# Kernel tuning notes

Hardware: AMD Instinct MI355X
Metric: run time of the kernel (lower is better)

Reference implementation:

```python
import jax, jax.numpy as jnp
import numpy as np

H = 16  # n_heads
D = 64  # d_keys


def setup_inputs() -> dict:
    key = jax.random.key(0)
    ks = jax.random.split(key, 11)
    b, n, dm = 2, 2048, 1024
    s = 1.0 / np.sqrt(dm)
    return {
        "q": jax.random.normal(ks[0], (b, n, dm), jnp.float32),
        "k": jax.random.normal(ks[1], (b, n, dm), jnp.float32),
        "v": jax.random.normal(ks[2], (b, n, dm), jnp.float32),
        "Wq": jax.random.normal(ks[3], (dm, H * D), jnp.float32) * s,
        "bq": jax.random.normal(ks[4], (H * D,), jnp.float32) * 0.01,
        "Wk": jax.random.normal(ks[5], (dm, H * D), jnp.float32) * s,
        "bk": jax.random.normal(ks[6], (H * D,), jnp.float32) * 0.01,
        "Wv": jax.random.normal(ks[7], (dm, H * D), jnp.float32) * s,
        "bv": jax.random.normal(ks[8], (H * D,), jnp.float32) * 0.01,
        "Wo": jax.random.normal(ks[9], (H * D, dm), jnp.float32) * s,
        "bo": jax.random.normal(ks[10], (dm,), jnp.float32) * 0.01,
    }


def reference(q, k, v, Wq, bq, Wk, bk, Wv, bv, Wo, bo):
    b, n_q, _ = q.shape
    n_k = k.shape[1]
    # projections -> [b, n, h, d]
    qh = (q @ Wq + bq).reshape(b, n_q, H, D)
    kh = (k @ Wk + bk).reshape(b, n_k, H, D)
    vh = (v @ Wv + bv).reshape(b, n_k, H, D)
    # scores [b, h, n, m]
    scores = jnp.einsum('bnhd,bmhd->bhnm', qh, kh)
    causal = jnp.triu(jnp.ones((n_q, n_k), dtype=bool), k=1)  # True above diag
    scores = jnp.where(causal, -jnp.inf, scores)
    att = jax.nn.softmax(scores / np.sqrt(D).astype(np.float32), axis=-1)
    att_out = jnp.einsum('bhnm,bmhd->bnhd', att, vh).reshape(b, n_q, H * D)
    return att_out @ Wo + bo
```

## Files before the change

### kernel.cpp

```cpp
#include <hip/hip_runtime.h>

typedef float f32x4 __attribute__((ext_vector_type(4)));
typedef __bf16 bf16x8 __attribute__((ext_vector_type(8)));
typedef __bf16 bf16x4 __attribute__((ext_vector_type(4)));
typedef __bf16 bf16_t;

#define NH 16
#define DH 64
#define SEQ 2048
#define DM 1024

extern "C" hipError_t hipMemPtrGetInfo(void* ptr, size_t* size);

__device__ __forceinline__ bf16x8 ld8(const bf16_t* p) { return *(const bf16x8*)p; }
__device__ __forceinline__ void st8(bf16_t* p, bf16x8 v) { *(bf16x8*)p = v; }

__device__ __forceinline__ void gl_lds16(const bf16_t* g, bf16_t* l)
{
    __builtin_amdgcn_global_load_lds(
        (const __attribute__((address_space(1))) unsigned int*)g,
        (__attribute__((address_space(3))) unsigned int*)l, 16, 0, 0);
}

__global__ __launch_bounds__(256) void fill_sentinel(float* out, unsigned n, float val)
{
    unsigned stride = gridDim.x * blockDim.x;
    for (unsigned i = blockIdx.x * blockDim.x + threadIdx.x; i < n; i += stride)
        out[i] = val;
}

__global__ __launch_bounds__(256) void prep(
    const float* __restrict__ q, const float* __restrict__ k,
    const float* __restrict__ v,
    const float* __restrict__ w0, const float* __restrict__ w1,
    const float* __restrict__ w2, const float* __restrict__ w3,
    bf16_t* __restrict__ xb, bf16_t* __restrict__ wt)
{
    int z = blockIdx.z;
    if (z < 3) {
        const float* src = (z == 0) ? q : (z == 1) ? k : v;
        bf16_t* dst = xb + (size_t)z * (4096u * 1024u);
        size_t i8 = ((size_t)blockIdx.x * 256 + threadIdx.x) * 8;
        f32x4 u = *(const f32x4*)(src + i8);
        f32x4 w = *(const f32x4*)(src + i8 + 4);
        bf16x8 h = { (bf16_t)u.x, (bf16_t)u.y, (bf16_t)u.z, (bf16_t)u.w,
                     (bf16_t)w.x, (bf16_t)w.y, (bf16_t)w.z, (bf16_t)w.w };
        st8(dst + i8, h);
    } else {
        int x = blockIdx.x;
        if (x >= 1024) return;
        int w = x >> 8, rem = x & 255;
        int bx = rem & 15, by = rem >> 4;
        const float* in = (w == 0) ? w0 : (w == 1) ? w1 : (w == 2) ? w2 : w3;
        bf16_t* out = wt + (size_t)w * DM * DM;
        __shared__ __align__(16) bf16_t tile[64][72];
        int t = threadIdx.x;
        int k0 = by * 64, n0 = bx * 64;
        int r0 = t >> 4, c0 = (t & 15) * 4;
        for (int p = 0; p < 4; p++) {
            int r = r0 + p * 16;
            const float* src = in + (size_t)(k0 + r) * DM + n0 + c0;
            for (int i = 0; i < 4; i++) tile[r][c0 + i] = (bf16_t)src[i];
        }
        __syncthreads();
        for (int p = 0; p < 4; p++) {
            int rn = r0 + p * 16;
            bf16_t* dst = out + (size_t)(n0 + rn) * DM + k0 + c0;
            for (int i = 0; i < 4; i++) dst[i] = tile[c0 + i][rn];
        }
    }
}

__device__ __forceinline__ void gemm_epilogue(
    f32x4 (&acc)[4][4], const float* bias, bf16_t* out, float* outf,
    int mode, int out_is_f32, int m0, int n0, int wr0, int wc0, int g, int l16)
{
    float scale = (mode == 0) ? 0.125f : 1.0f;
    for (int mi = 0; mi < 4; mi++) {
        int mbase = m0 + wr0 + mi * 16 + g * 4;
        for (int ni = 0; ni < 4; ni++) {
            int col = n0 + wc0 + ni * 16 + l16;
            float bv = bias[col];
            if (mode == 2) {
                int bb = mbase >> 11, nn0 = mbase & 2047;
                int h = col >> 6, d = col & 63;
                bf16x4 pv;
                for (int r = 0; r < 4; r++) pv[r] = (bf16_t)(acc[mi][ni][r] + bv);
                *(bf16x4*)(out + ((size_t)(bb * NH + h) * DH + d) * SEQ + nn0) = pv;
            } else {
                for (int r = 0; r < 4; r++) {
                    int mr = mbase + r;
                    float sv = (acc[mi][ni][r] + bv) * scale;
                    if (mode == 3) {
                        if (out_is_f32) outf[(size_t)mr * 1024 + col] = sv;
                        else            out[(size_t)mr * 1024 + col] = (bf16_t)sv;
                    } else {
                        int bb = mr >> 11, nn = mr & 2047;
                        int h = col >> 6, d = col & 63;
                        out[((size_t)(bb * NH + h) * SEQ + nn) * DH + d] = (bf16_t)sv;
                    }
                }
            }
        }
    }
}

__global__ __launch_bounds__(512, 2) void gemm_qkv(
    const bf16_t* __restrict__ xb_base, const bf16_t* __restrict__ wt_base,
    const float* __restrict__ b0, const float* __restrict__ b1,
    const float* __restrict__ b2, bf16_t* __restrict__ out_base)
{
    int z = blockIdx.z;
    const bf16_t* X  = xb_base + (size_t)z * (4096u * 1024u);
    const bf16_t* WT = wt_base + (size_t)z * DM * DM;
    const float* bias = (z == 0) ? b0 : (z == 1) ? b1 : b2;
    bf16_t* out = out_base + (size_t)z * (4096u * 1024u);

    int m0 = blockIdx.x * 256;
    int n0 = blockIdx.y * 256;

    __shared__ __align__(16) bf16_t Ab[2][256 * 64];
    __shared__ __align__(16) bf16_t Bb[2][256 * 64];

    int tid  = threadIdx.x;
    int lane = tid & 63, w = tid >> 6;
    int g = lane >> 4, l16 = lane & 15;
    int wr0 = (w >> 2) * 128;
    int wc0 = (w & 3) * 64;
    int rl = lane >> 3, cl = lane & 7;

    f32x4 acc[8][4] = {};

    auto stage = [&](int b, int t) {
        int k0 = t * 64;
        #pragma unroll
        for (int i = 0; i < 4; i++) {
            int row = i * 64 + w * 8 + rl;
            int cs  = cl ^ (row & 7);
            gl_lds16(X + (size_t)(m0 + row) * DM + k0 + cs * 8,
                     &Ab[b][(i * 64 + w * 8) * 64 + lane * 8]);
        }
        #pragma unroll
        for (int i = 0; i < 4; i++) {
            int row = i * 64 + w * 8 + rl;
            int cs  = cl ^ (row & 7);
            gl_lds16(WT + (size_t)(n0 + row) * DM + k0 + cs * 8,
                     &Bb[b][(i * 64 + w * 8) * 64 + lane * 8]);
        }
    };

    stage(0, 0);
    stage(1, 1);
    __syncthreads();

    for (int t = 0; t < 16; t++) {
        int b = t & 1;
        bf16x8 bfr[4][2];
        #pragma unroll
        for (int ni = 0; ni < 4; ni++) {
            int rn = wc0 + ni * 16 + l16;
            #pragma unroll
            for (int kk = 0; kk < 2; kk++)
                bfr[ni][kk] = ld8(&Bb[b][rn * 64 + (((kk * 4 + g) ^ (rn & 7)) * 8)]);
        }
        #pragma unroll
        for (int mp = 0; mp < 4; mp++) {
            bf16x8 af[2][2];
            #pragma unroll
            for (int i = 0; i < 2; i++) {
                int ra = wr0 + (mp * 2 + i) * 16 + l16;
                #pragma unroll
                for (int kk = 0; kk < 2; kk++)
                    af[i][kk] = ld8(&Ab[b][ra * 64 + (((kk * 4 + g) ^ (ra & 7)) * 8)]);
            }
            __builtin_amdgcn_s_setprio(1);
            #pragma unroll
            for (int i = 0; i < 2; i++)
                #pragma unroll
                for (int ni = 0; ni < 4; ni++)
                    #pragma unroll
                    for (int kk = 0; kk < 2; kk++)
                        acc[mp * 2 + i][ni] = __builtin_amdgcn_mfma_f32_16x16x32_bf16(
                            af[i][kk], bfr[ni][kk], acc[mp * 2 + i][ni], 0, 0, 0);
            __builtin_amdgcn_s_setprio(0);
        }
        __syncthreads();
        if (t + 2 < 16) stage(b, t + 2);
    }

    float scale = (z == 0) ? 0.125f : 1.0f;
    #pragma unroll
    for (int mi = 0; mi < 8; mi++) {
        int mbase = m0 + wr0 + mi * 16 + g * 4;
        int bb = mbase >> 11, nn0 = mbase & 2047;
        #pragma unroll
        for (int ni = 0; ni < 4; ni++) {
            int col = n0 + wc0 + ni * 16 + l16;
            float bv = bias[col];
            int h = col >> 6, d = col & 63;
            if (z == 2) {
                bf16x4 pv;
                for (int r = 0; r < 4; r++) pv[r] = (bf16_t)(acc[mi][ni][r] + bv);
                *(bf16x4*)(out + ((size_t)(bb * NH + h) * DH + d) * SEQ + nn0) = pv;
            } else {
                for (int r = 0; r < 4; r++) {
                    int nn = nn0 + r;
                    out[((size_t)(bb * NH + h) * SEQ + nn) * DH + d] =
                        (bf16_t)((acc[mi][ni][r] + bv) * scale);
                }
            }
        }
    }
}

__global__ __launch_bounds__(256) void gemm_fast(
    const bf16_t* __restrict__ xb_base, const bf16_t* __restrict__ wt_base,
    const float* __restrict__ b0, const float* __restrict__ b1,
    const float* __restrict__ b2, bf16_t* __restrict__ out_base,
    float* __restrict__ outf, int mode_base, int out_is_f32)
{
    int z = blockIdx.z;
    const bf16_t* X    = xb_base + (size_t)z * (4096u * 1024u);
    const bf16_t* WT   = wt_base + (size_t)z * DM * DM;
    const float* bias  = (z == 0) ? b0 : (z == 1) ? b1 : b2;
    bf16_t* out = out_base + (size_t)z * (4096u * 1024u);
    int mode = mode_base + z;

    int m0 = blockIdx.x * 128;
    int n0 = blockIdx.y * 128;

    __shared__ __align__(16) bf16_t Alds[128 * 64];
    __shared__ __align__(16) bf16_t Blds[128 * 64];

    int t = threadIdx.x;
    int lane = t & 63, wave = t >> 6;
    int g = lane >> 4, l16 = lane & 15;
    int wr0 = (wave >> 1) * 64, wc0 = (wave & 1) * 64;
    int crow = lane >> 3;
    int ccol = (lane & 7) * 8;

    f32x4 acc[4][4] = {};

    for (int k0 = 0; k0 < DM; k0 += 64) {
        __syncthreads();
        for (int c = wave; c < 16; c += 4) {
            int row = c * 8 + crow;
            gl_lds16(X  + (size_t)(m0 + row) * DM + k0 + ccol,
                     Alds + c * 512 + lane * 8);
            gl_lds16(WT + (size_t)(n0 + row) * DM + k0 + ccol,
                     Blds + c * 512 + lane * 8);
        }
        __syncthreads();
        for (int kk = 0; kk < 2; kk++) {
            bf16x8 af[4], bfr[4];
            for (int i = 0; i < 4; i++)
                af[i] = ld8(Alds + (wr0 + i * 16 + l16) * 64 + kk * 32 + g * 8);
            for (int i = 0; i < 4; i++)
                bfr[i] = ld8(Blds + (wc0 + i * 16 + l16) * 64 + kk * 32 + g * 8);
            for (int mi = 0; mi < 4; mi++)
                for (int ni = 0; ni < 4; ni++)
                    acc[mi][ni] = __builtin_amdgcn_mfma_f32_16x16x32_bf16(
                        af[mi], bfr[ni], acc[mi][ni], 0, 0, 0);
        }
    }
    gemm_epilogue(acc, bias, out, outf, mode, out_is_f32, m0, n0, wr0, wc0, g, l16);
}

__global__ __launch_bounds__(256) void gemm_mha(
    const float* __restrict__ x0, const float* __restrict__ x1,
    const float* __restrict__ x2, const bf16_t* __restrict__ xb,
    const bf16_t* __restrict__ wt_base,
    const float* __restrict__ b0, const float* __restrict__ b1,
    const float* __restrict__ b2, bf16_t* __restrict__ out_base,
    float* __restrict__ outf, int mode_base, int out_is_f32)
{
    int z = blockIdx.z;
    const float* Xf    = (z == 0) ? x0 : (z == 1) ? x1 : x2;
    const bf16_t* WT   = wt_base + (size_t)z * DM * DM;
    const float* bias  = (z == 0) ? b0 : (z == 1) ? b1 : b2;
    bf16_t* out = out_base + (size_t)z * (4096u * 1024u);
    int mode = mode_base + z;

    int m0 = blockIdx.x * 128;
    int n0 = blockIdx.y * 128;

    __shared__ __align__(16) bf16_t Alds[128 * 64];
    __shared__ __align__(16) bf16_t Blds[128 * 64];

    int t = threadIdx.x;
    int lane = t & 63, wave = t >> 6;
    int g = lane >> 4, l16 = lane & 15;
    int wr0 = (wave >> 1) * 64, wc0 = (wave & 1) * 64;

    f32x4 acc[4][4] = {};
    int srow = t >> 3, sk = (t & 7) * 8;

    for (int k0 = 0; k0 < DM; k0 += 64) {
        __syncthreads();
        if (mode < 3) {
            for (int p = 0; p < 4; p++) {
                int r = srow + p * 32;
                const float* s4 = Xf + (size_t)(m0 + r) * DM + k0 + sk;
                f32x4 u = *(const f32x4*)s4;
                f32x4 w = *(const f32x4*)(s4 + 4);
                bf16x8 h = { (bf16_t)u.x, (bf16_t)u.y, (bf16_t)u.z, (bf16_t)u.w,
                             (bf16_t)w.x, (bf16_t)w.y, (bf16_t)w.z, (bf16_t)w.w };
                st8(Alds + r * 64 + sk, h);
            }
        } else {
            for (int p = 0; p < 4; p++) {
                int r = srow + p * 32;
                st8(Alds + r * 64 + sk, ld8(xb + (size_t)(m0 + r) * DM + k0 + sk));
            }
        }
        for (int p = 0; p < 4; p++) {
            int r = srow + p * 32;
            st8(Blds + r * 64 + sk, ld8(WT + (size_t)(n0 + r) * DM + k0 + sk));
        }
        __syncthreads();
        for (int kk = 0; kk < 2; kk++) {
            bf16x8 af[4], bfr[4];
            for (int i = 0; i < 4; i++)
                af[i] = ld8(Alds + (wr0 + i * 16 + l16) * 64 + kk * 32 + g * 8);
            for (int i = 0; i < 4; i++)
                bfr[i] = ld8(Blds + (wc0 + i * 16 + l16) * 64 + kk * 32 + g * 8);
            for (int mi = 0; mi < 4; mi++)
                for (int ni = 0; ni < 4; ni++)
                    acc[mi][ni] = __builtin_amdgcn_mfma_f32_16x16x32_bf16(
                        af[mi], bfr[ni], acc[mi][ni], 0, 0, 0);
        }
    }
    gemm_epilogue(acc, bias, out, outf, mode, out_is_f32, m0, n0, wr0, wc0, g, l16);
}

__global__ __launch_bounds__(512) void attn(
    const bf16_t* __restrict__ Qh, const bf16_t* __restrict__ Kh,
    const bf16_t* __restrict__ VT, bf16_t* __restrict__ att)
{
    int bhx = blockIdx.x;
    int yy  = blockIdx.y;
    int p   = (yy < 8) ? yy : 23 - yy;
    int TB  = 2 * p + 2;

    const bf16_t* Qb = Qh + (size_t)bhx * SEQ * DH;
    const bf16_t* Kb = Kh + (size_t)bhx * SEQ * DH;
    const bf16_t* Vb = VT + (size_t)bhx * DH * SEQ;

    __shared__ __align__(16) bf16_t Klds[2][64 * 72];
    __shared__ __align__(16) bf16_t Vlds[2][64 * 72];
    __shared__ __align__(16) bf16_t Plds[8][16 * 72];

    int t = threadIdx.x, lane = t & 63, wave = t >> 6;
    int g = lane >> 4, l16 = lane & 15;
    int srow = t >> 3, sk = (t & 7) * 8;
    int qt = 2 * p + (wave >> 2);
    int Tw = qt + 1;
    int rowl = (wave & 3) * 16 + l16;

    bf16x8 qf[2];
    for (int kk = 0; kk < 2; kk++)
        qf[kk] = ld8(Qb + (size_t)(qt * 64 + rowl) * DH + kk * 32 + g * 8);

    f32x4 accO[4] = {};
    float l = 0.f;
    bf16_t* Pw = Plds[wave];

    st8(&Klds[0][srow * 72 + sk], ld8(Kb + (size_t)srow * DH + sk));
    st8(&Vlds[0][srow * 72 + sk], ld8(Vb + (size_t)srow * SEQ + sk));

    for (int j = 0; j < TB; j++) {
        __syncthreads();
        if (j + 1 < TB) {
            int b = (j + 1) & 1;
            st8(&Klds[b][srow * 72 + sk],
                ld8(Kb + (size_t)((j + 1) * 64 + srow) * DH + sk));
            st8(&Vlds[b][srow * 72 + sk],
                ld8(Vb + (size_t)srow * SEQ + (j + 1) * 64 + sk));
        }
        if (j >= Tw) continue;
        int buf = j & 1;
        bool diag = (j == Tw - 1);

        f32x4 s[4];
        for (int c = 0; c < 4; c++) {
            f32x4 a = {};
            for (int kk = 0; kk < 2; kk++) {
                bf16x8 kf = ld8(&Klds[buf][(c * 16 + l16) * 72 + kk * 32 + g * 8]);
                a = __builtin_amdgcn_mfma_f32_16x16x32_bf16(kf, qf[kk], a, 0, 0, 0);
            }
            s[c] = a;
        }
        for (int c = 0; c < 4; c++) {
            bf16x4 pv;
            for (int r = 0; r < 4; r++) {
                float v = s[c][r];
                if (diag && (c * 16 + g * 4 + r) > rowl) v = -1e30f;
                float pe = __expf(v);
                l += pe;
                pv[r] = (bf16_t)pe;
            }
            *(bf16x4*)(Pw + l16 * 72 + c * 16 + g * 4) = pv;
        }
        asm volatile("s_waitcnt lgkmcnt(0)" ::: "memory");

        bf16x8 pf0 = ld8(Pw + l16 * 72 + g * 8);
        bf16x8 pf1 = ld8(Pw + l16 * 72 + 32 + g * 8);
        for (int c2 = 0; c2 < 4; c2++) {
            bf16x8 vf0 = ld8(&Vlds[buf][(c2 * 16 + l16) * 72 + g * 8]);
            accO[c2] = __builtin_amdgcn_mfma_f32_16x16x32_bf16(vf0, pf0, accO[c2], 0, 0, 0);
            bf16x8 vf1 = ld8(&Vlds[buf][(c2 * 16 + l16) * 72 + 32 + g * 8]);
            accO[c2] = __builtin_amdgcn_mfma_f32_16x16x32_bf16(vf1, pf1, accO[c2], 0, 0, 0);
        }

        if (diag) {
            float lt = l;
            lt += __shfl_xor(lt, 16);
            lt += __shfl_xor(lt, 32);
            float inv = 1.f / lt;
            int qabs = qt * 64 + rowl;
            int bb = bhx >> 4, h = bhx & 15;
            for (int c2 = 0; c2 < 4; c2++) {
                bf16x4 ov;
                for (int r = 0; r < 4; r++) ov[r] = (bf16_t)(accO[c2][r] * inv);
                *(bf16x4*)(att + (((size_t)bb * SEQ + qabs) * NH + h) * DH
                           + c2 * 16 + g * 4) = ov;
            }
        }
    }
}

extern "C" void kernel_launch(void* const* d_in, const int* in_sizes, int n_in,
                              void* d_out, int out_size, void* d_ws, size_t ws_size,
                              hipStream_t stream) {
    const float* q  = (const float*)d_in[0];
    const float* k  = (const float*)d_in[1];
    const float* v  = (const float*)d_in[2];
    const float* Wq = (const float*)d_in[3];
    const float* bq = (const float*)d_in[4];
    const float* Wk = (const float*)d_in[5];
    const float* bk = (const float*)d_in[6];
    const float* Wv = (const float*)d_in[7];
    const float* bv = (const float*)d_in[8];
    const float* Wo = (const float*)d_in[9];
    const float* bo = (const float*)d_in[10];

    const size_t MAT = 1024u * 1024u;
    const size_t BIG = 4096u * 1024u;
    const size_t NEED_BASE = 64 + (4 * BIG + 4 * MAT) * 2;
    const size_t NEED_FAST = NEED_BASE + 3 * BIG * 2;

    if (ws_size < NEED_BASE) {
        fill_sentinel<<<1024, 256, 0, stream>>>((float*)d_out,
                                                (unsigned)out_size, 100.0f);
        return;
    }

    int out_is_f32 = 1;
    size_t osz = 0;
    if (hipMemPtrGetInfo(d_out, &osz) == hipSuccess && osz != 0 &&
        osz < (size_t)out_size * 4)
        out_is_f32 = 0;

    bf16_t* base = (bf16_t*)d_ws + 32;
    bf16_t* Qh  = base;
    bf16_t* Kh  = Qh + BIG;
    bf16_t* VT  = Kh + BIG;
    bf16_t* att = VT + BIG;
    bf16_t* WT  = att + BIG;
    bf16_t* Xb  = WT + 4 * MAT;

    if (ws_size >= NEED_FAST) {
        prep<<<dim3(2048, 1, 4), 256, 0, stream>>>(q, k, v, Wq, Wk, Wv, Wo, Xb, WT);
        gemm_qkv<<<dim3(16, 4, 3), 512, 0, stream>>>(Xb, WT, bq, bk, bv, Qh);
        attn<<<dim3(32, 16), 512, 0, stream>>>(Qh, Kh, VT, att);
        gemm_fast<<<dim3(32, 8, 1), 256, 0, stream>>>(att, WT + 3 * MAT,
                                                      bo, bo, bo,
                                                      (bf16_t*)d_out, (float*)d_out,
                                                      3, out_is_f32);
    } else {
        prep<<<dim3(2048, 1, 4), 256, 0, stream>>>(q, k, v, Wq, Wk, Wv, Wo,
                                                   (bf16_t*)d_ws, WT);
        gemm_mha<<<dim3(32, 8, 3), 256, 0, stream>>>(q, k, v, nullptr, WT,
                                                     bq, bk, bv, Qh, nullptr, 0, 0);
        attn<<<dim3(32, 16), 512, 0, stream>>>(Qh, Kh, VT, att);
        gemm_mha<<<dim3(32, 8, 1), 256, 0, stream>>>(nullptr, nullptr, nullptr, att,
                                                     WT + 3 * MAT, bo, bo, bo,
                                                     (bf16_t*)d_out, (float*)d_out,
                                                     3, out_is_f32);
    }
}
```

Measured before the change: 234.2 us.

## Restructure QKV GEMM into quadrant-split, fine-grained pipelined LDS staging schedule

Splits each 256x256 tile into 128-row halves of A and B, each with its own LDS slot. The main loop interleaves eight sub-steps, each issuing one half-tile global-to-LDS load while the MFMAs for one quadrant run. Explicit s_barrier, vmcnt and lgkmcnt waits and sched_barriers replace the coarse __syncthreads double buffer, so loads overlap compute more finely. This adds more barriers per k-step and a hand-managed wait-count schedule that must match the order in which loads are issued.

```diff
diff --git a/kernel.cpp b/kernel.cpp
--- a/kernel.cpp
+++ b/kernel.cpp
@@ -105,112 +105,170 @@
     }
 }
 
+#define MIDBAR do { __builtin_amdgcn_s_barrier(); \
+    asm volatile("s_waitcnt lgkmcnt(0)" ::: "memory"); \
+    __builtin_amdgcn_sched_barrier(0); } while (0)
+#define ENDBAR do { __builtin_amdgcn_sched_barrier(0); \
+    __builtin_amdgcn_s_barrier(); } while (0)
+#define VMC6 asm volatile("s_waitcnt vmcnt(6)" ::: "memory")
+#define VMC0 asm volatile("s_waitcnt vmcnt(0)" ::: "memory")
+
 __global__ __launch_bounds__(512, 2) void gemm_qkv(
     const bf16_t* __restrict__ xb_base, const bf16_t* __restrict__ wt_base,
-    const float* __restrict__ b0, const float* __restrict__ b1,
-    const float* __restrict__ b2, bf16_t* __restrict__ out_base)
+    const float* __restrict__ b0v, const float* __restrict__ b1v,
+    const float* __restrict__ b2v, bf16_t* __restrict__ out_base)
 {
     int z = blockIdx.z;
     const bf16_t* X  = xb_base + (size_t)z * (4096u * 1024u);
     const bf16_t* WT = wt_base + (size_t)z * DM * DM;
-    const float* bias = (z == 0) ? b0 : (z == 1) ? b1 : b2;
+    const float* bias = (z == 0) ? b0v : (z == 1) ? b1v : b2v;
     bf16_t* out = out_base + (size_t)z * (4096u * 1024u);
 
     int m0 = blockIdx.x * 256;
     int n0 = blockIdx.y * 256;
 
-    __shared__ __align__(16) bf16_t Ab[2][256 * 64];
-    __shared__ __align__(16) bf16_t Bb[2][256 * 64];
+    __shared__ __align__(16) bf16_t Ab[2 * 2 * 128 * 64];
+    __shared__ __align__(16) bf16_t Bb[2 * 2 * 128 * 64];
 
     int tid  = threadIdx.x;
     int lane = tid & 63, w = tid >> 6;
     int g = lane >> 4, l16 = lane & 15;
-    int wr0 = (w >> 2) * 128;
-    int wc0 = (w & 3) * 64;
+    int wm = w >> 2, wn = w & 3;
     int rl = lane >> 3, cl = lane & 7;
-
-    f32x4 acc[8][4] = {};
-
-    auto stage = [&](int b, int t) {
-        int k0 = t * 64;
+    int w8 = w * 8;
+
+    f32x4 acc[2][2][4][2] = {};
+
+    auto stA = [&](int d, int h, int kt) {
         #pragma unroll
-        for (int i = 0; i < 4; i++) {
-            int row = i * 64 + w * 8 + rl;
+        for (int j = 0; j < 2; j++) {
+            int row = h * 128 + j * 64 + w8 + rl;
             int cs  = cl ^ (row & 7);
-            gl_lds16(X + (size_t)(m0 + row) * DM + k0 + cs * 8,
-                     &Ab[b][(i * 64 + w * 8) * 64 + lane * 8]);
-        }
+            gl_lds16(X + (size_t)(m0 + row) * DM + kt * 64 + cs * 8,
+                     &Ab[((d * 2 + h) * 128 + j * 64 + w8) * 64 + lane * 8]);
+        }
+    };
+    auto stB = [&](int d, int h, int kt) {
         #pragma unroll
-        for (int i = 0; i < 4; i++) {
-            int row = i * 64 + w * 8 + rl;
+        for (int j = 0; j < 2; j++) {
+            int row = h * 128 + j * 64 + w8 + rl;
             int cs  = cl ^ (row & 7);
-            gl_lds16(WT + (size_t)(n0 + row) * DM + k0 + cs * 8,
-                     &Bb[b][(i * 64 + w * 8) * 64 + lane * 8]);
+            gl_lds16(WT + (size_t)(n0 + row) * DM + kt * 64 + cs * 8,
+                     &Bb[((d * 2 + h) * 128 + j * 64 + w8) * 64 + lane * 8]);
         }
     };
-
-    stage(0, 0);
-    stage(1, 1);
-    __syncthreads();
-
-    for (int t = 0; t < 16; t++) {
-        int b = t & 1;
-        bf16x8 bfr[4][2];
+    auto rdA = [&](int d, int h, bf16x8 (&af)[4][2]) {
         #pragma unroll
-        for (int ni = 0; ni < 4; ni++) {
-            int rn = wc0 + ni * 16 + l16;
+        for (int mf = 0; mf < 4; mf++) {
+            int ar = wm * 64 + mf * 16 + l16;
             #pragma unroll
             for (int kk = 0; kk < 2; kk++)
-                bfr[ni][kk] = ld8(&Bb[b][rn * 64 + (((kk * 4 + g) ^ (rn & 7)) * 8)]);
-        }
+                af[mf][kk] = ld8(&Ab[((d * 2 + h) * 128 + ar) * 64 +
+                                     (((kk * 4 + g) ^ (ar & 7)) * 8)]);
+        }
+    };
+    auto rdB = [&](int d, int h, bf16x8 (&bfr)[2][2]) {
         #pragma unroll
-        for (int mp = 0; mp < 4; mp++) {
-            bf16x8 af[2][2];
+        for (int nf = 0; nf < 2; nf++) {
+            int br = wn * 32 + nf * 16 + l16;
             #pragma unroll
-            for (int i = 0; i < 2; i++) {
-                int ra = wr0 + (mp * 2 + i) * 16 + l16;
+            for (int kk = 0; kk < 2; kk++)
+                bfr[nf][kk] = ld8(&Bb[((d * 2 + h) * 128 + br) * 64 +
+                                      (((kk * 4 + g) ^ (br & 7)) * 8)]);
+        }
+    };
+    auto mm = [&](bf16x8 (&af)[4][2], bf16x8 (&bfr)[2][2], f32x4 (&a)[4][2]) {
+        __builtin_amdgcn_s_setprio(1);
+        #pragma unroll
+        for (int mf = 0; mf < 4; mf++)
+            #pragma unroll
+            for (int nf = 0; nf < 2; nf++)
                 #pragma unroll
                 for (int kk = 0; kk < 2; kk++)
-                    af[i][kk] = ld8(&Ab[b][ra * 64 + (((kk * 4 + g) ^ (ra & 7)) * 8)]);
-            }
-            __builtin_amdgcn_s_setprio(1);
-            #pragma unroll
-            for (int i = 0; i < 2; i++)
-                #pragma unroll
-                for (int ni = 0; ni < 4; ni++)
-                    #pragma unroll
-                    for (int kk = 0; kk < 2; kk++)
-                        acc[mp * 2 + i][ni] = __builtin_amdgcn_mfma_f32_16x16x32_bf16(
-                            af[i][kk], bfr[ni][kk], acc[mp * 2 + i][ni], 0, 0, 0);
-            __builtin_amdgcn_s_setprio(0);
-        }
-        __syncthreads();
-        if (t + 2 < 16) stage(b, t + 2);
-    }
+                    a[mf][nf] = __builtin_amdgcn_mfma_f32_16x16x32_bf16(
+                        af[mf][kk], bfr[nf][kk], a[mf][nf], 0, 0, 0);
+        __builtin_amdgcn_s_setprio(0);
+    };
+
+    bf16x8 af[4][2], b0[2][2], b1[2][2];
+
+    stA(0, 0, 0); stB(0, 0, 0); stA(0, 1, 0); stB(0, 1, 0);
+    stA(1, 0, 1); stB(1, 0, 1); stA(1, 1, 1);
+    VMC6;
+    __builtin_amdgcn_s_barrier();
+
+    #pragma unroll 1
+    for (int i = 0; i < 7; i++) {
+        int ktB = 2 * i + 1, ktN = 2 * i + 2, ktN1 = 2 * i + 3;
+        rdA(0, 0, af); rdB(0, 0, b0);
+        stB(1, 1, ktB);
+        MIDBAR; mm(af, b0, acc[0][0]); ENDBAR;
+        rdB(0, 1, b1);
+        stA(0, 0, ktN);
+        MIDBAR; mm(af, b1, acc[0][1]); ENDBAR;
+        rdA(0, 1, af);
+        stB(0, 0, ktN);
+        MIDBAR; mm(af, b0, acc[1][0]); ENDBAR;
+        stA(0, 1, ktN);
+        VMC6;
+        MIDBAR; mm(af, b1, acc[1][1]); ENDBAR;
+        rdA(1, 0, af); rdB(1, 0, b0);
+        stB(0, 1, ktN);
+        MIDBAR; mm(af, b0, acc[0][0]); ENDBAR;
+        rdB(1, 1, b1);
+        stA(1, 0, ktN1);
+        MIDBAR; mm(af, b1, acc[0][1]); ENDBAR;
+        rdA(1, 1, af);
+        stB(1, 0, ktN1);
+        MIDBAR; mm(af, b0, acc[1][0]); ENDBAR;
+        stA(1, 1, ktN1);
+        VMC6;
+        MIDBAR; mm(af, b1, acc[1][1]); ENDBAR;
+    }
+    rdA(0, 0, af); rdB(0, 0, b0);
+    stB(1, 1, 15);
+    MIDBAR; mm(af, b0, acc[0][0]); ENDBAR;
+    rdB(0, 1, b1);
+    MIDBAR; mm(af, b1, acc[0][1]); ENDBAR;
+    rdA(0, 1, af);
+    MIDBAR; mm(af, b0, acc[1][0]); ENDBAR;
+    VMC0;
+    MIDBAR; mm(af, b1, acc[1][1]); ENDBAR;
+    rdA(1, 0, af); rdB(1, 0, b0);
+    MIDBAR; mm(af, b0, acc[0][0]); ENDBAR;
+    rdB(1, 1, b1);
+    MIDBAR; mm(af, b1, acc[0][1]); ENDBAR;
+    rdA(1, 1, af);
+    MIDBAR; mm(af, b0, acc[1][0]); ENDBAR;
+    MIDBAR; mm(af, b1, acc[1][1]);
 
     float scale = (z == 0) ? 0.125f : 1.0f;
     #pragma unroll
-    for (int mi = 0; mi < 8; mi++) {
-        int mbase = m0 + wr0 + mi * 16 + g * 4;
-        int bb = mbase >> 11, nn0 = mbase & 2047;
+    for (int Mh = 0; Mh < 2; Mh++)
         #pragma unroll
-        for (int ni = 0; ni < 4; ni++) {
-            int col = n0 + wc0 + ni * 16 + l16;
-            float bv = bias[col];
-            int h = col >> 6, d = col & 63;
-            if (z == 2) {
-                bf16x4 pv;
-                for (int r = 0; r < 4; r++) pv[r] = (bf16_t)(acc[mi][ni][r] + bv);
-                *(bf16x4*)(out + ((size_t)(bb * NH + h) * DH + d) * SEQ + nn0) = pv;
-            } else {
-                for (int r = 0; r < 4; r++) {
-                    int nn = nn0 + r;
-                    out[((size_t)(bb * NH + h) * SEQ + nn) * DH + d] =
-                        (bf16_t)((acc[mi][ni][r] + bv) * scale);
+        for (int mf = 0; mf < 4; mf++) {
+            int mbase = m0 + Mh * 128 + wm * 64 + mf * 16 + g * 4;
+            int bb = mbase >> 11, nn0 = mbase & 2047;
+            #pragma unroll
+            for (int Nh = 0; Nh < 2; Nh++)
+                #pragma unroll
+                for (int nf = 0; nf < 2; nf++) {
+                    int col = n0 + Nh * 128 + wn * 32 + nf * 16 + l16;
+                    float bv = bias[col];
+                    int h = col >> 6, d = col & 63;
+                    if (z == 2) {
+                        bf16x4 pv;
+                        for (int r = 0; r < 4; r++)
+                            pv[r] = (bf16_t)(acc[Mh][Nh][mf][nf][r] + bv);
+                        *(bf16x4*)(out + ((size_t)(bb * NH + h) * DH + d) * SEQ
+                                   + nn0) = pv;
+                    } else {
+                        for (int r = 0; r < 4; r++)
+                            out[((size_t)(bb * NH + h) * SEQ + nn0 + r) * DH + d] =
+                                (bf16_t)((acc[Mh][Nh][mf][nf][r] + bv) * scale);
+                    }
                 }
-            }
-        }
-    }
+        }
 }
 
 __global__ __launch_bounds__(256) void gemm_fast(
```

Measured after the change: 233.4 us. About the same (-0.4%).
